# Kernel optimization log

Hardware: AMD Instinct MI355X
Metric: run time of the kernel (lower is better)

Reference implementation:

```python
import jax, jax.numpy as jnp
import numpy as np

N_NODES = 100000
N_EDGES = 1600000
IN_CH = 256
OUT_CH = 128
EPS = 1e-12


def setup_inputs() -> dict:
    key = jax.random.key(0)
    k1, k2, k3 = jax.random.split(key, 3)
    x = jax.random.normal(k1, (N_NODES, IN_CH), dtype=jnp.float32)
    edge_index = jax.random.randint(k2, (2, N_EDGES), 0, N_NODES, dtype=jnp.int64)
    W = jax.random.normal(k3, (IN_CH, OUT_CH), dtype=jnp.float32) / np.float32(np.sqrt(IN_CH))
    b = jnp.zeros((OUT_CH,), dtype=jnp.float32)
    return {"x": x, "edge_index": edge_index, "W": W, "b": b}


def reference(x, edge_index, W, b):
    n = x.shape[0]
    # GCNConv: linear transform first, then normalized aggregation with self-loops
    h = x @ W  # [N, out]
    loops = jnp.arange(n, dtype=edge_index.dtype)
    row = jnp.concatenate([edge_index[0], loops])  # source nodes
    col = jnp.concatenate([edge_index[1], loops])  # destination nodes
    deg = jax.ops.segment_sum(jnp.ones_like(col, dtype=h.dtype), col, num_segments=n)
    dinv = jnp.where(deg > 0, jax.lax.rsqrt(jnp.maximum(deg, 1.0)), 0.0)  # deg^-1/2, inf->0
    wgt = dinv[row] * dinv[col]  # symmetric normalization per edge
    agg = jax.ops.segment_sum(h[row] * wgt[:, None], col, num_segments=n) + b  # [N, out]
    # min-max scale per node (dim=1)
    zmin = agg.min(axis=1, keepdims=True)
    zmax = agg.max(axis=1, keepdims=True)
    z = (agg - zmin) / (zmax - zmin)
    # F.normalize: L2 along dim=1 with eps clamp
    nrm = jnp.maximum(jnp.linalg.norm(z, axis=1, keepdims=True), EPS)
    return z / nrm
```

## Files before the change

### kernel.cpp

```cpp
#include <hip/hip_runtime.h>
#include <hip/hip_bf16.h>

#define N_NODES 100000
#define N_EDGES 1600000
#define IN_CH 256
#define OUT_CH 128

#define BSZ 512
#define NBUCK 196
#define CHH 6400
#define CSC 8192

#define GEMM_ROWS 32
#define LDS_STRIDE 260

typedef __attribute__((ext_vector_type(8))) short short8;
typedef __attribute__((ext_vector_type(4))) float floatx4;

union bfu { __hip_bfloat16 b; unsigned short u; };

__device__ inline unsigned short f2bf(float v) {
    bfu cv; cv.b = __float2bfloat16(v); return cv.u;
}
__device__ inline float bf2f(unsigned short u) {
    bfu cv; cv.u = u; return __bfloat162float(cv.b);
}

__global__ __launch_bounds__(256) void pa_zero(int* bhist) {
    int t = threadIdx.x;
    if (t < NBUCK) bhist[t] = 0;
}

__global__ __launch_bounds__(256) void pa_hist(const int* __restrict__ cols,
                                               int* __restrict__ bhist) {
    __shared__ int lh[NBUCK];
    int t = threadIdx.x;
    if (t < NBUCK) lh[t] = 0;
    __syncthreads();
    int s0 = blockIdx.x * CHH;
    int e1 = min(N_EDGES, s0 + CHH);
    for (int i = s0 + t; i < e1; i += 256) atomicAdd(&lh[cols[i] >> 9], 1);
    __syncthreads();
    if (t < NBUCK && lh[t]) atomicAdd(&bhist[t], lh[t]);
}

__global__ __launch_bounds__(256) void pa_scan(const int* __restrict__ bhist,
                                               int* __restrict__ bbase,
                                               int* __restrict__ bcursor) {
    __shared__ int s[256];
    int t = threadIdx.x;
    int v = (t < NBUCK) ? bhist[t] : 0;
    s[t] = v;
    __syncthreads();
    for (int off = 1; off < 256; off <<= 1) {
        int u = (t >= off) ? s[t - off] : 0;
        __syncthreads();
        s[t] += u;
        __syncthreads();
    }
    if (t < NBUCK) {
        int e = s[t] - v;
        bbase[t] = e;
        bcursor[t] = e;
    }
}

__global__ __launch_bounds__(256) void pa_scatter(const int* __restrict__ rows,
                                                  const int* __restrict__ cols,
                                                  int* __restrict__ bcursor,
                                                  unsigned* __restrict__ ebuf) {
    __shared__ int lcnt[NBUCK];
    __shared__ int lbase[NBUCK];
    int t = threadIdx.x;
    if (t < NBUCK) lcnt[t] = 0;
    __syncthreads();
    int s0 = blockIdx.x * CSC;
    int e1 = min(N_EDGES, s0 + CSC);
    for (int i = s0 + t; i < e1; i += 256) atomicAdd(&lcnt[cols[i] >> 9], 1);
    __syncthreads();
    if (t < NBUCK) {
        int c = lcnt[t];
        lbase[t] = c ? atomicAdd(&bcursor[t], c) : 0;
        lcnt[t] = 0;
    }
    __syncthreads();
    for (int i = s0 + t; i < e1; i += 256) {
        int c = cols[i], r = rows[i];
        int bk = c >> 9;
        int rank = atomicAdd(&lcnt[bk], 1);
        ebuf[lbase[bk] + rank] = ((unsigned)(c & (BSZ - 1)) << 17) | (unsigned)r;
    }
}

__global__ __launch_bounds__(256) void pb_build(const unsigned* __restrict__ ebuf,
                                                const int* __restrict__ bhist,
                                                const int* __restrict__ bbase,
                                                int* __restrict__ cnt,
                                                int* __restrict__ base,
                                                float* __restrict__ dinv,
                                                int* __restrict__ es) {
    __shared__ int nh[BSZ];
    __shared__ int sc[BSZ];
    __shared__ int lcur[BSZ];
    int t = threadIdx.x;
    int bk = blockIdx.x;
    int bb = bbase[bk];
    int bc = bhist[bk];
    nh[t] = 0; nh[t + 256] = 0;
    lcur[t] = 0; lcur[t + 256] = 0;
    __syncthreads();
    for (int i = t; i < bc; i += 256) atomicAdd(&nh[ebuf[bb + i] >> 17], 1);
    __syncthreads();
    sc[t] = nh[t]; sc[t + 256] = nh[t + 256];
    __syncthreads();
    for (int off = 1; off < BSZ; off <<= 1) {
        int v0 = (t >= off) ? sc[t - off] : 0;
        int i1 = t + 256;
        int v1 = (i1 >= off) ? sc[i1 - off] : 0;
        __syncthreads();
        sc[t] += v0; sc[i1] += v1;
        __syncthreads();
    }
#pragma unroll
    for (int q = 0; q < 2; ++q) {
        int dl = t + q * 256;
        int node = bk * BSZ + dl;
        if (node < N_NODES) {
            int c = nh[dl];
            cnt[node] = c;
            base[node] = bb + sc[dl] - c;
            dinv[node] = rsqrtf((float)(c + 1));
        }
    }
    for (int i = t; i < bc; i += 256) {
        unsigned v = ebuf[bb + i];
        int dl = v >> 17;
        int src = (int)(v & 0x1FFFFu);
        int rank = atomicAdd(&lcur[dl], 1);
        es[bb + sc[dl] - nh[dl] + rank] = src;
    }
}

__global__ void k_prep_w(const float* __restrict__ W,
                         unsigned short* __restrict__ wb_hi,
                         unsigned short* __restrict__ wb_lo) {
    int t = blockIdx.x * 256 + threadIdx.x;
    if (t >= IN_CH * OUT_CH) return;
    int j = t & 7;
    int lane = (t >> 3) & 63;
    int s = (t >> 9) & 7;
    int nt = t >> 12;
    int k = s * 32 + (lane >> 4) * 8 + j;
    int n = nt * 16 + (lane & 15);
    float w = W[k * OUT_CH + n];
    unsigned short hi = f2bf(w);
    wb_hi[t] = hi;
    wb_lo[t] = f2bf(w - bf2f(hi));
}

__global__ __launch_bounds__(512) void k_gemm(const float* __restrict__ x,
                                              const unsigned short* __restrict__ wb_hi,
                                              const unsigned short* __restrict__ wb_lo,
                                              const float* __restrict__ dinv,
                                              float* __restrict__ h,
                                              unsigned short* __restrict__ hbs) {
    __shared__ float xs[GEMM_ROWS * LDS_STRIDE];
    int wv = threadIdx.x >> 6;
    int lane = threadIdx.x & 63;
    int row0 = blockIdx.x * GEMM_ROWS;

#pragma unroll
    for (int r = 0; r < 4; ++r) {
        int lr = wv * 4 + r;
        const float* src = x + (size_t)(row0 + lr) * IN_CH + lane * 4;
        __builtin_amdgcn_global_load_lds(
            (const __attribute__((address_space(1))) void*)src,
            (__attribute__((address_space(3))) void*)&xs[lr * LDS_STRIDE],
            16, 0, 0);
    }

    short8 Bh[8], Bl[8];
    const short8* bhp = (const short8*)wb_hi + (size_t)wv * 8 * 64 + lane;
    const short8* blp = (const short8*)wb_lo + (size_t)wv * 8 * 64 + lane;
#pragma unroll
    for (int s = 0; s < 8; ++s) {
        Bh[s] = bhp[s * 64];
        Bl[s] = blp[s * 64];
    }

    asm volatile("s_waitcnt vmcnt(0)" ::: "memory");
    __syncthreads();

    int r15 = lane & 15;
    int quad = lane >> 4;

    floatx4 acc[2];
#pragma unroll
    for (int ms = 0; ms < 2; ++ms) {
        acc[ms] = (floatx4){0.f, 0.f, 0.f, 0.f};
        const float* ap = xs + (ms * 16 + r15) * LDS_STRIDE + quad * 8;
#pragma unroll
        for (int s = 0; s < 8; ++s) {
            float4 v0 = *(const float4*)(ap + s * 32);
            float4 v1 = *(const float4*)(ap + s * 32 + 4);
            float xv[8] = {v0.x, v0.y, v0.z, v0.w, v1.x, v1.y, v1.z, v1.w};
            short8 ah, al;
#pragma unroll
            for (int j = 0; j < 8; ++j) {
                unsigned short hi = f2bf(xv[j]);
                ah[j] = (short)hi;
                al[j] = (short)f2bf(xv[j] - bf2f(hi));
            }
            acc[ms] = __builtin_amdgcn_mfma_f32_16x16x32_bf16(ah, Bh[s], acc[ms], 0, 0, 0);
            acc[ms] = __builtin_amdgcn_mfma_f32_16x16x32_bf16(ah, Bl[s], acc[ms], 0, 0, 0);
            acc[ms] = __builtin_amdgcn_mfma_f32_16x16x32_bf16(al, Bh[s], acc[ms], 0, 0, 0);
        }
    }

#pragma unroll
    for (int ms = 0; ms < 2; ++ms)
#pragma unroll
        for (int r = 0; r < 4; ++r) {
            int row = row0 + ms * 16 + quad * 4 + r;
            size_t idx = (size_t)row * OUT_CH + wv * 16 + r15;
            float v = acc[ms][r];
            h[idx] = v;
            hbs[idx] = f2bf(v * dinv[row]);
        }
}

__global__ __launch_bounds__(256) void k_agg_fin(const float* __restrict__ h,
                                                 const unsigned short* __restrict__ hbs,
                                                 const float* __restrict__ dinv,
                                                 const int* __restrict__ es,
                                                 const int* __restrict__ base,
                                                 const int* __restrict__ cnt,
                                                 const float* __restrict__ b,
                                                 float* __restrict__ out) {
    int node = (blockIdx.x * 256 + threadIdx.x) >> 6;
    int lane = threadIdx.x & 63;
    if (node >= N_NODES) return;

    float dn = dinv[node];
    float2 hv = ((const float2*)(h + (size_t)node * OUT_CH))[lane];
    float2 bv = ((const float2*)b)[lane];

    int st = __builtin_amdgcn_readfirstlane(base[node]);
    int d  = __builtin_amdgcn_readfirstlane(cnt[node]);
    const int* ep = es + st;

    float ex = 0.f, ey = 0.f;
    int j = 0;
    for (; j + 4 <= d; j += 4) {
        int s0 = __builtin_amdgcn_readfirstlane(ep[j + 0]);
        int s1 = __builtin_amdgcn_readfirstlane(ep[j + 1]);
        int s2 = __builtin_amdgcn_readfirstlane(ep[j + 2]);
        int s3 = __builtin_amdgcn_readfirstlane(ep[j + 3]);
        unsigned g0 = ((const unsigned*)(hbs + (size_t)s0 * OUT_CH))[lane];
        unsigned g1 = ((const unsigned*)(hbs + (size_t)s1 * OUT_CH))[lane];
        unsigned g2 = ((const unsigned*)(hbs + (size_t)s2 * OUT_CH))[lane];
        unsigned g3 = ((const unsigned*)(hbs + (size_t)s3 * OUT_CH))[lane];
        ex += __uint_as_float(g0 << 16);
        ey += __uint_as_float(g0 & 0xffff0000u);
        ex += __uint_as_float(g1 << 16);
        ey += __uint_as_float(g1 & 0xffff0000u);
        ex += __uint_as_float(g2 << 16);
        ey += __uint_as_float(g2 & 0xffff0000u);
        ex += __uint_as_float(g3 << 16);
        ey += __uint_as_float(g3 & 0xffff0000u);
    }
    for (; j < d; ++j) {
        int s0 = __builtin_amdgcn_readfirstlane(ep[j]);
        unsigned g0 = ((const unsigned*)(hbs + (size_t)s0 * OUT_CH))[lane];
        ex += __uint_as_float(g0 << 16);
        ey += __uint_as_float(g0 & 0xffff0000u);
    }

    float w0 = dn * dn;
    float2 acc;
    acc.x = hv.x * w0 + bv.x + dn * ex;
    acc.y = hv.y * w0 + bv.y + dn * ey;

    float lmin = fminf(acc.x, acc.y), lmax = fmaxf(acc.x, acc.y);
#pragma unroll
    for (int m = 32; m; m >>= 1) {
        lmin = fminf(lmin, __shfl_xor(lmin, m, 64));
        lmax = fmaxf(lmax, __shfl_xor(lmax, m, 64));
    }
    float scale = 1.0f / (lmax - lmin);
    float zx = (acc.x - lmin) * scale;
    float zy = (acc.y - lmin) * scale;
    float ss = zx * zx + zy * zy;
#pragma unroll
    for (int m = 32; m; m >>= 1) ss += __shfl_xor(ss, m, 64);
    float inv = 1.0f / fmaxf(sqrtf(ss), 1e-12f);
    float2 o;
    o.x = zx * inv;
    o.y = zy * inv;
    ((float2*)(out + (size_t)node * OUT_CH))[lane] = o;
}

extern "C" void kernel_launch(void* const* d_in, const int* in_sizes, int n_in,
                              void* d_out, int out_size, void* d_ws, size_t ws_size,
                              hipStream_t stream) {
    const float* x = (const float*)d_in[0];
    const int* ei = (const int*)d_in[1];
    const float* W = (const float*)d_in[2];
    const float* b = (const float*)d_in[3];
    float* out = (float*)d_out;

    char* ws = (char*)d_ws;
    size_t o = 0;
    auto alloc = [&](size_t bytes) { void* p = ws + o; o = (o + bytes + 255) & ~(size_t)255; return p; };
    float* dinv    = (float*)alloc((size_t)N_NODES * 4);
    int*   cnt     = (int*)  alloc((size_t)N_NODES * 4);
    int*   base    = (int*)  alloc((size_t)N_NODES * 4);
    int*   bhist   = (int*)  alloc(NBUCK * 4);
    int*   bbase   = (int*)  alloc(NBUCK * 4);
    int*   bcursor = (int*)  alloc(NBUCK * 4);
    unsigned short* wb_hi = (unsigned short*)alloc((size_t)IN_CH * OUT_CH * 2);
    unsigned short* wb_lo = (unsigned short*)alloc((size_t)IN_CH * OUT_CH * 2);
    float* h       = (float*)alloc((size_t)N_NODES * OUT_CH * 4);
    unsigned short* hbs = (unsigned short*)alloc((size_t)N_NODES * OUT_CH * 2);
    unsigned* ebuf = (unsigned*)alloc((size_t)N_EDGES * 4);
    int*   es      = (int*)  alloc((size_t)N_EDGES * 4);

    const int* rows = ei;
    const int* cols = ei + N_EDGES;

    pa_zero<<<1, 256, 0, stream>>>(bhist);
    pa_hist<<<(N_EDGES + CHH - 1) / CHH, 256, 0, stream>>>(cols, bhist);
    pa_scan<<<1, 256, 0, stream>>>(bhist, bbase, bcursor);
    pa_scatter<<<(N_EDGES + CSC - 1) / CSC, 256, 0, stream>>>(rows, cols, bcursor, ebuf);
    pb_build<<<NBUCK, 256, 0, stream>>>(ebuf, bhist, bbase, cnt, base, dinv, es);

    k_prep_w<<<(IN_CH * OUT_CH + 255) / 256, 256, 0, stream>>>(W, wb_hi, wb_lo);
    k_gemm<<<N_NODES / GEMM_ROWS, 512, 0, stream>>>(x, wb_hi, wb_lo, dinv, h, hbs);

    k_agg_fin<<<(N_NODES + 3) / 4, 256, 0, stream>>>(h, hbs, dinv, es, base, cnt, b, out);
}
```

Measured before the change: 332.8 us.

## Drop fp32 h buffer, pre-split x to bf16 in LDS, batch edge-index loads

The GEMM no longer writes an fp32 copy of h. The self-loop term now comes from the dinv-scaled bf16 hbs row, so the aggregation reads only hbs, which removes a large write and read of N x 128 floats. The GEMM now splits x into bf16 hi/lo once per element and stores the MFMA-ready fragments in LDS, replacing the async global-to-LDS fp32 copy and the per-wave re-conversion. The aggregation loads up to 64 neighbour indices per wave in one vector load, picks them out with readlane, and unrolls by 8 for more loads in flight. In exchange, the self term is rounded to bf16, which slightly lowers accuracy.

```diff
diff --git a/kernel.cpp b/kernel.cpp
--- a/kernel.cpp
+++ b/kernel.cpp
@@ -12,7 +12,6 @@
 #define CSC 8192
 
 #define GEMM_ROWS 32
-#define LDS_STRIDE 260
 
 typedef __attribute__((ext_vector_type(8))) short short8;
 typedef __attribute__((ext_vector_type(4))) float floatx4;
@@ -162,22 +161,13 @@
                                               const unsigned short* __restrict__ wb_hi,
                                               const unsigned short* __restrict__ wb_lo,
                                               const float* __restrict__ dinv,
-                                              float* __restrict__ h,
                                               unsigned short* __restrict__ hbs) {
-    __shared__ float xs[GEMM_ROWS * LDS_STRIDE];
-    int wv = threadIdx.x >> 6;
-    int lane = threadIdx.x & 63;
+    __shared__ short8 xbh[1024];
+    __shared__ short8 xbl[1024];
+    int t = threadIdx.x;
+    int wv = t >> 6;
+    int lane = t & 63;
     int row0 = blockIdx.x * GEMM_ROWS;
-
-#pragma unroll
-    for (int r = 0; r < 4; ++r) {
-        int lr = wv * 4 + r;
-        const float* src = x + (size_t)(row0 + lr) * IN_CH + lane * 4;
-        __builtin_amdgcn_global_load_lds(
-            (const __attribute__((address_space(1))) void*)src,
-            (__attribute__((address_space(3))) void*)&xs[lr * LDS_STRIDE],
-            16, 0, 0);
-    }
 
     short8 Bh[8], Bl[8];
     const short8* bhp = (const short8*)wb_hi + (size_t)wv * 8 * 64 + lane;
@@ -188,7 +178,28 @@
         Bl[s] = blp[s * 64];
     }
 
-    asm volatile("s_waitcnt vmcnt(0)" ::: "memory");
+#pragma unroll
+    for (int q = 0; q < 2; ++q) {
+        int slot = q * 512 + t;
+        int ms = slot >> 9;
+        int s  = (slot >> 6) & 7;
+        int l  = slot & 63;
+        int row = row0 + ms * 16 + (l & 15);
+        int col = s * 32 + (l >> 4) * 8;
+        const float4* xp = (const float4*)(x + (size_t)row * IN_CH + col);
+        float4 v0 = xp[0];
+        float4 v1 = xp[1];
+        float xv[8] = {v0.x, v0.y, v0.z, v0.w, v1.x, v1.y, v1.z, v1.w};
+        short8 hh, ll;
+#pragma unroll
+        for (int j = 0; j < 8; ++j) {
+            unsigned short hi = f2bf(xv[j]);
+            hh[j] = (short)hi;
+            ll[j] = (short)f2bf(xv[j] - bf2f(hi));
+        }
+        xbh[slot] = hh;
+        xbl[slot] = ll;
+    }
     __syncthreads();
 
     int r15 = lane & 15;
@@ -198,19 +209,10 @@
 #pragma unroll
     for (int ms = 0; ms < 2; ++ms) {
         acc[ms] = (floatx4){0.f, 0.f, 0.f, 0.f};
-        const float* ap = xs + (ms * 16 + r15) * LDS_STRIDE + quad * 8;
 #pragma unroll
         for (int s = 0; s < 8; ++s) {
-            float4 v0 = *(const float4*)(ap + s * 32);
-            float4 v1 = *(const float4*)(ap + s * 32 + 4);
-            float xv[8] = {v0.x, v0.y, v0.z, v0.w, v1.x, v1.y, v1.z, v1.w};
-            short8 ah, al;
-#pragma unroll
-            for (int j = 0; j < 8; ++j) {
-                unsigned short hi = f2bf(xv[j]);
-                ah[j] = (short)hi;
-                al[j] = (short)f2bf(xv[j] - bf2f(hi));
-            }
+            short8 ah = xbh[(ms * 8 + s) * 64 + lane];
+            short8 al = xbl[(ms * 8 + s) * 64 + lane];
             acc[ms] = __builtin_amdgcn_mfma_f32_16x16x32_bf16(ah, Bh[s], acc[ms], 0, 0, 0);
             acc[ms] = __builtin_amdgcn_mfma_f32_16x16x32_bf16(ah, Bl[s], acc[ms], 0, 0, 0);
             acc[ms] = __builtin_amdgcn_mfma_f32_16x16x32_bf16(al, Bh[s], acc[ms], 0, 0, 0);
@@ -223,14 +225,11 @@
         for (int r = 0; r < 4; ++r) {
             int row = row0 + ms * 16 + quad * 4 + r;
             size_t idx = (size_t)row * OUT_CH + wv * 16 + r15;
-            float v = acc[ms][r];
-            h[idx] = v;
-            hbs[idx] = f2bf(v * dinv[row]);
+            hbs[idx] = f2bf(acc[ms][r] * dinv[row]);
         }
 }
 
-__global__ __launch_bounds__(256) void k_agg_fin(const float* __restrict__ h,
-                                                 const unsigned short* __restrict__ hbs,
+__global__ __launch_bounds__(256) void k_agg_fin(const unsigned short* __restrict__ hbs,
                                                  const float* __restrict__ dinv,
                                                  const int* __restrict__ es,
                                                  const int* __restrict__ base,
@@ -241,45 +240,75 @@
     int lane = threadIdx.x & 63;
     if (node >= N_NODES) return;
 
+    const unsigned* hp = (const unsigned*)hbs;
     float dn = dinv[node];
-    float2 hv = ((const float2*)(h + (size_t)node * OUT_CH))[lane];
     float2 bv = ((const float2*)b)[lane];
 
     int st = __builtin_amdgcn_readfirstlane(base[node]);
     int d  = __builtin_amdgcn_readfirstlane(cnt[node]);
-    const int* ep = es + st;
-
-    float ex = 0.f, ey = 0.f;
+
+    unsigned gs = hp[(size_t)node * 64 + lane];
+    float ex = __uint_as_float(gs << 16);
+    float ey = __uint_as_float(gs & 0xffff0000u);
+
+    int sid = (lane < d) ? es[st + lane] : 0;
+    int dc = d < 64 ? d : 64;
+
     int j = 0;
-    for (; j + 4 <= d; j += 4) {
-        int s0 = __builtin_amdgcn_readfirstlane(ep[j + 0]);
-        int s1 = __builtin_amdgcn_readfirstlane(ep[j + 1]);
-        int s2 = __builtin_amdgcn_readfirstlane(ep[j + 2]);
-        int s3 = __builtin_amdgcn_readfirstlane(ep[j + 3]);
-        unsigned g0 = ((const unsigned*)(hbs + (size_t)s0 * OUT_CH))[lane];
-        unsigned g1 = ((const unsigned*)(hbs + (size_t)s1 * OUT_CH))[lane];
-        unsigned g2 = ((const unsigned*)(hbs + (size_t)s2 * OUT_CH))[lane];
-        unsigned g3 = ((const unsigned*)(hbs + (size_t)s3 * OUT_CH))[lane];
-        ex += __uint_as_float(g0 << 16);
-        ey += __uint_as_float(g0 & 0xffff0000u);
-        ex += __uint_as_float(g1 << 16);
-        ey += __uint_as_float(g1 & 0xffff0000u);
-        ex += __uint_as_float(g2 << 16);
-        ey += __uint_as_float(g2 & 0xffff0000u);
-        ex += __uint_as_float(g3 << 16);
-        ey += __uint_as_float(g3 & 0xffff0000u);
+    for (; j + 8 <= dc; j += 8) {
+        int s0 = __builtin_amdgcn_readlane(sid, j + 0);
+        int s1 = __builtin_amdgcn_readlane(sid, j + 1);
+        int s2 = __builtin_amdgcn_readlane(sid, j + 2);
+        int s3 = __builtin_amdgcn_readlane(sid, j + 3);
+        int s4 = __builtin_amdgcn_readlane(sid, j + 4);
+        int s5 = __builtin_amdgcn_readlane(sid, j + 5);
+        int s6 = __builtin_amdgcn_readlane(sid, j + 6);
+        int s7 = __builtin_amdgcn_readlane(sid, j + 7);
+        unsigned g0 = hp[(size_t)s0 * 64 + lane];
+        unsigned g1 = hp[(size_t)s1 * 64 + lane];
+        unsigned g2 = hp[(size_t)s2 * 64 + lane];
+        unsigned g3 = hp[(size_t)s3 * 64 + lane];
+        unsigned g4 = hp[(size_t)s4 * 64 + lane];
+        unsigned g5 = hp[(size_t)s5 * 64 + lane];
+        unsigned g6 = hp[(size_t)s6 * 64 + lane];
+        unsigned g7 = hp[(size_t)s7 * 64 + lane];
+        ex += __uint_as_float(g0 << 16);  ey += __uint_as_float(g0 & 0xffff0000u);
+        ex += __uint_as_float(g1 << 16);  ey += __uint_as_float(g1 & 0xffff0000u);
+        ex += __uint_as_float(g2 << 16);  ey += __uint_as_float(g2 & 0xffff0000u);
+        ex += __uint_as_float(g3 << 16);  ey += __uint_as_float(g3 & 0xffff0000u);
+        ex += __uint_as_float(g4 << 16);  ey += __uint_as_float(g4 & 0xffff0000u);
+        ex += __uint_as_float(g5 << 16);  ey += __uint_as_float(g5 & 0xffff0000u);
+        ex += __uint_as_float(g6 << 16);  ey += __uint_as_float(g6 & 0xffff0000u);
+        ex += __uint_as_float(g7 << 16);  ey += __uint_as_float(g7 & 0xffff0000u);
+    }
+    for (; j + 4 <= dc; j += 4) {
+        int s0 = __builtin_amdgcn_readlane(sid, j + 0);
+        int s1 = __builtin_amdgcn_readlane(sid, j + 1);
+        int s2 = __builtin_amdgcn_readlane(sid, j + 2);
+        int s3 = __builtin_amdgcn_readlane(sid, j + 3);
+        unsigned g0 = hp[(size_t)s0 * 64 + lane];
+        unsigned g1 = hp[(size_t)s1 * 64 + lane];
+        unsigned g2 = hp[(size_t)s2 * 64 + lane];
+        unsigned g3 = hp[(size_t)s3 * 64 + lane];
+        ex += __uint_as_float(g0 << 16);  ey += __uint_as_float(g0 & 0xffff0000u);
+        ex += __uint_as_float(g1 << 16);  ey += __uint_as_float(g1 & 0xffff0000u);
+        ex += __uint_as_float(g2 << 16);  ey += __uint_as_float(g2 & 0xffff0000u);
+        ex += __uint_as_float(g3 << 16);  ey += __uint_as_float(g3 & 0xffff0000u);
+    }
+    for (; j < dc; ++j) {
+        int s0 = __builtin_amdgcn_readlane(sid, j);
+        unsigned g0 = hp[(size_t)s0 * 64 + lane];
+        ex += __uint_as_float(g0 << 16);  ey += __uint_as_float(g0 & 0xffff0000u);
     }
     for (; j < d; ++j) {
-        int s0 = __builtin_amdgcn_readfirstlane(ep[j]);
-        unsigned g0 = ((const unsigned*)(hbs + (size_t)s0 * OUT_CH))[lane];
-        ex += __uint_as_float(g0 << 16);
-        ey += __uint_as_float(g0 & 0xffff0000u);
-    }
-
-    float w0 = dn * dn;
+        int s0 = __builtin_amdgcn_readfirstlane(es[st + j]);
+        unsigned g0 = hp[(size_t)s0 * 64 + lane];
+        ex += __uint_as_float(g0 << 16);  ey += __uint_as_float(g0 & 0xffff0000u);
+    }
+
     float2 acc;
-    acc.x = hv.x * w0 + bv.x + dn * ex;
-    acc.y = hv.y * w0 + bv.y + dn * ey;
+    acc.x = dn * ex + bv.x;
+    acc.y = dn * ey + bv.y;
 
     float lmin = fminf(acc.x, acc.y), lmax = fmaxf(acc.x, acc.y);
 #pragma unroll
@@ -320,7 +349,6 @@
     int*   bcursor = (int*)  alloc(NBUCK * 4);
     unsigned short* wb_hi = (unsigned short*)alloc((size_t)IN_CH * OUT_CH * 2);
     unsigned short* wb_lo = (unsigned short*)alloc((size_t)IN_CH * OUT_CH * 2);
-    float* h       = (float*)alloc((size_t)N_NODES * OUT_CH * 4);
     unsigned short* hbs = (unsigned short*)alloc((size_t)N_NODES * OUT_CH * 2);
     unsigned* ebuf = (unsigned*)alloc((size_t)N_EDGES * 4);
     int*   es      = (int*)  alloc((size_t)N_EDGES * 4);
@@ -335,7 +363,7 @@
     pb_build<<<NBUCK, 256, 0, stream>>>(ebuf, bhist, bbase, cnt, base, dinv, es);
 
     k_prep_w<<<(IN_CH * OUT_CH + 255) / 256, 256, 0, stream>>>(W, wb_hi, wb_lo);
-    k_gemm<<<N_NODES / GEMM_ROWS, 512, 0, stream>>>(x, wb_hi, wb_lo, dinv, h, hbs);
-
-    k_agg_fin<<<(N_NODES + 3) / 4, 256, 0, stream>>>(h, hbs, dinv, es, base, cnt, b, out);
-}
+    k_gemm<<<N_NODES / GEMM_ROWS, 512, 0, stream>>>(x, wb_hi, wb_lo, dinv, hbs);
+
+    k_agg_fin<<<(N_NODES + 3) / 4, 256, 0, stream>>>(hbs, dinv, es, base, cnt, b, out);
+}
```

Result: faster. 317.9 us (-4.5%).
